# Kernel tuning notes

Hardware: AMD Instinct MI355X
Metric: run time of the kernel (lower is better)

The kernel has to match this reference:

```python
import jax, jax.numpy as jnp
import numpy as np

# dims matching init_kwargs
B, C, T = 64, 8, 2048
K, DIL = 16, 4            # kernel_size, dilation
MLP = 16                  # mlp_dim
NF = min(MLP, K // 2 + 1) # n_frequencies = 9
FEAT = C * NF * 2         # 144
H1, H2 = 64, 32           # ReLUBlock hidden dims (64 -> 64//2)
EFF = DIL * (K - 1)       # 60
W = T - EFF               # 1988 windows


def setup_inputs() -> dict:
    key = jax.random.key(0)
    ks = jax.random.split(key, 10)
    def lin(k, out_d, in_d):
        kw, kb = jax.random.split(k)
        bound = 1.0 / np.sqrt(in_d)
        w = jax.random.uniform(kw, (out_d, in_d), jnp.float32, -bound, bound)
        b = jax.random.uniform(kb, (out_d,), jnp.float32, -bound, bound)
        return w, b
    x = jax.random.normal(ks[0], (B, C, T), jnp.float32)
    proj_w, proj_b = lin(ks[1], MLP, FEAT)
    w1, b1 = lin(ks[2], H1, MLP)
    w2, b2 = lin(ks[3], H2, H1)
    out_w, out_b = lin(ks[4], 1, H2)
    agg_w = jax.random.normal(ks[5], (W,), jnp.float32) * 0.1
    return {"x": x, "proj_w": proj_w, "proj_b": proj_b, "w1": w1, "b1": b1,
            "w2": w2, "b2": b2, "out_w": out_w, "out_b": out_b, "agg_w": agg_w}


def reference(x, proj_w, proj_b, w1, b1, w2, b2, out_w, out_b, agg_w):
    # Build all dilated windows at once: window[t, j] = x[..., t - (K-1-j)*DIL]
    starts = jnp.arange(EFF, T)                      # [W]
    offs = -(K - 1 - jnp.arange(K)) * DIL            # [K]
    idx = starts[:, None] + offs[None, :]            # [W, K]
    win = x[:, :, idx]                               # [B, C, W, K]
    f = jnp.fft.rfft(win, axis=-1)[..., :NF]         # [B, C, W, NF]
    mag = jnp.log1p(jnp.abs(f))
    ph = jnp.angle(f) / jnp.pi
    feat = jnp.stack([mag, ph], axis=-1)             # [B, C, W, NF, 2]
    feat = feat.transpose(0, 2, 1, 3, 4).reshape(B, W, FEAT)  # [B, W, C*NF*2]
    p = jnp.tanh(feat @ proj_w.T + proj_b) * jnp.pi  # [B, W, MLP]
    h = jax.nn.relu(p @ w1.T + b1)                   # [B, W, H1]
    h = jax.nn.relu(h @ w2.T + b2)                   # [B, W, H2]
    out = (h @ out_w.T + out_b)[..., 0]              # [B, W]
    wts = jax.nn.softmax(agg_w)                      # [W]
    return (out * wts[None, :]).sum(axis=1)          # [B]
```

## Files before the change

### kernel.cpp

```cpp
#include <hip/hip_runtime.h>
#include <math.h>

#define B_    64
#define C_    8
#define T_    2048
#define K_    16
#define NF_   9
#define FEAT_ 144
#define MLP_  16
#define H1_   64
#define H2_   32
#define EFF_  60
#define W_    1988
#define NCHK_ 32
#define PI_F  3.14159265358979323846f
#define SPW   36
#define S1    20
#define S2    36

constexpr float COS16[16] = {
   1.0f,  0.92387953251128674f,  0.70710678118654752f,  0.38268343236508977f,
   0.0f, -0.38268343236508977f, -0.70710678118654752f, -0.92387953251128674f,
  -1.0f, -0.92387953251128674f, -0.70710678118654752f, -0.38268343236508977f,
   0.0f,  0.38268343236508977f,  0.70710678118654752f,  0.92387953251128674f };
constexpr float SIN16F[16] = {
   0.0f,  0.38268343236508977f,  0.70710678118654752f,  0.92387953251128674f,
   1.0f,  0.92387953251128674f,  0.70710678118654752f,  0.38268343236508977f,
   0.0f, -0.38268343236508977f, -0.70710678118654752f, -0.92387953251128674f,
  -1.0f, -0.92387953251128674f, -0.70710678118654752f, -0.38268343236508977f };

__device__ __forceinline__ float fast_log1p(float s) {
  return __builtin_amdgcn_logf(1.0f + s) * 0.69314718055994531f;
}

__device__ __forceinline__ float atanpi_poly(float r) {
  const float s2 = r * r;
  float p = -0.0037310f;
  p = fmaf(p, s2,  0.0167600f);
  p = fmaf(p, s2, -0.0370617f);
  p = fmaf(p, s2,  0.0616068f);
  p = fmaf(p, s2, -0.10587734f);
  p = fmaf(p, s2,  0.31830265f);
  return r * p;
}

__device__ __forceinline__ float atan2pi_fast(float im, float re) {
  const float ax = fabsf(re), ay = fabsf(im);
  const float mx = fmaxf(ax, ay), mn = fminf(ax, ay);
  const float r = mn * __builtin_amdgcn_rcpf(fmaxf(mx, 1e-37f));
  float t = atanpi_poly(r);
  t = (ay > ax) ? 0.5f - t : t;
  t = (__float_as_uint(re) & 0x80000000u) ? 1.0f - t : t;
  return copysignf(t, im);
}

__device__ __forceinline__ float fast_tanh(float z) {
  const float az = fabsf(z);
  const float e = __builtin_amdgcn_exp2f(-2.8853900817779268f * az);
  const float th = fmaf(-2.0f, e * __builtin_amdgcn_rcpf(1.0f + e), 1.0f);
  return copysignf(th, z);
}

__global__ __launch_bounds__(256) void setup_kernel(const float* __restrict__ agg,
                                                    float* __restrict__ wts,
                                                    const float* __restrict__ pw,
                                                    const float* __restrict__ w2,
                                                    float* __restrict__ PWt,
                                                    float* __restrict__ W2t) {
  if (blockIdx.x == 0) {
    __shared__ float red[256];
    const int tid = threadIdx.x;
    float m = -INFINITY;
    for (int i = tid; i < W_; i += 256) m = fmaxf(m, agg[i]);
    red[tid] = m; __syncthreads();
    for (int s = 128; s > 0; s >>= 1) { if (tid < s) red[tid] = fmaxf(red[tid], red[tid+s]); __syncthreads(); }
    const float mx = red[0];
    __syncthreads();
    float sum = 0.f;
    for (int i = tid; i < W_; i += 256) sum += expf(agg[i] - mx);
    red[tid] = sum; __syncthreads();
    for (int s = 128; s > 0; s >>= 1) { if (tid < s) red[tid] += red[tid+s]; __syncthreads(); }
    const float inv = 1.f / red[0];
    for (int i = tid; i < W_; i += 256) wts[i] = expf(agg[i] - mx) * inv;
  } else {
    const int tid = (blockIdx.x - 1) * 256 + threadIdx.x;
    if (tid < MLP_ * FEAT_) {
      const int j = tid / FEAT_, f = tid - j * FEAT_;
      PWt[f * MLP_ + j] = pw[tid];
    }
    if (tid < H2_ * H1_) {
      const int m = tid >> 6, i = tid & 63;
      W2t[i * H2_ + m] = w2[tid];
    }
  }
}

__global__ __launch_bounds__(256) void tcn_fused(
    const float* __restrict__ x,
    const float* __restrict__ PWt, const float* __restrict__ proj_b,
    const float* __restrict__ w1, const float* __restrict__ b1,
    const float* __restrict__ W2t, const float* __restrict__ b2,
    const float* __restrict__ out_w, const float* __restrict__ out_b,
    const float* __restrict__ wts, float* __restrict__ partials) {
  __shared__ __align__(16) float PWl[72 * SPW];
  __shared__ __align__(16) float W1p[H1_ * S1];
  __shared__ __align__(16) float W2p[H1_ * S2];
  __shared__ float B1s[H1_];

  const int tid = threadIdx.x;
  for (int idx = tid; idx < 72 * 32; idx += 256) { const int r = idx >> 5, j = idx & 31; PWl[r * SPW + j] = PWt[idx]; }
  for (int idx = tid; idx < H1_ * MLP_; idx += 256) { const int i = idx >> 4, j = idx & 15; W1p[i * S1 + j] = w1[idx]; }
  for (int idx = tid; idx < H1_ * H2_; idx += 256) { const int i = idx >> 5, m = idx & 31; W2p[i * S2 + m] = W2t[idx]; }
  if (tid < H1_) B1s[tid] = b1[tid];
  __syncthreads();

  const int lane = tid & 63;
  const int wave = tid >> 6;
  const int wloc = lane & 15;
  const int sub  = lane >> 4;
  const int b     = blockIdx.y;
  const int chunk = blockIdx.x;
  const int w  = chunk * 64 + wave * 16 + wloc;
  const int wl = (w < W_) ? w : (W_ - 1);

  float pacc[MLP_];
  #pragma unroll
  for (int j = 0; j < MLP_; j++) pacc[j] = 0.f;

  #pragma unroll
  for (int cc = 0; cc < 2; cc++) {
    const int c = sub * 2 + cc;
    const float* xc = x + ((size_t)b * C_ + c) * T_ + wl;
    float win[K_];
    #pragma unroll
    for (int k = 0; k < K_; k++) win[k] = xc[k * 4];
    float ae[8], bo[8];
    #pragma unroll
    for (int k = 0; k < 8; k++) { ae[k] = win[k] + win[k+8]; bo[k] = win[k] - win[k+8]; }

    #pragma unroll
    for (int n = 0; n < NF_; n++) {
      float re = 0.f, im = 0.f;
      #pragma unroll
      for (int k = 0; k < 8; k++) {
        const float v = (n & 1) ? bo[k] : ae[k];
        const int t = (n * k) & 15;
        re = fmaf(v,  COS16[t],  re);
        im = fmaf(v, -SIN16F[t], im);
      }
      const float s   = __builtin_amdgcn_sqrtf(fmaf(re, re, im * im));
      const float mag = fast_log1p(s);
      const float ph  = atan2pi_fast(im, re);
      const float4* rmv = reinterpret_cast<const float4*>(&PWl[(c * NF_ + n) * SPW]);
      #pragma unroll
      for (int q = 0; q < 4; q++) {
        const float4 a  = rmv[q];
        const float4 bb = rmv[q + 4];
        pacc[4*q+0] = fmaf(mag, a.x, fmaf(ph, bb.x, pacc[4*q+0]));
        pacc[4*q+1] = fmaf(mag, a.y, fmaf(ph, bb.y, pacc[4*q+1]));
        pacc[4*q+2] = fmaf(mag, a.z, fmaf(ph, bb.z, pacc[4*q+2]));
        pacc[4*q+3] = fmaf(mag, a.w, fmaf(ph, bb.w, pacc[4*q+3]));
      }
    }
  }

  #pragma unroll
  for (int j = 0; j < MLP_; j++) {
    pacc[j] += __shfl_xor(pacc[j], 16, 64);
    pacc[j] += __shfl_xor(pacc[j], 32, 64);
  }
  float p[MLP_];
  #pragma unroll
  for (int j = 0; j < MLP_; j++) p[j] = fast_tanh(pacc[j] + proj_b[j]) * PI_F;

  float h2a[H2_];
  #pragma unroll
  for (int m = 0; m < H2_; m++) h2a[m] = 0.f;
  #pragma unroll 4
  for (int ii = 0; ii < 16; ii++) {
    const int i = sub + ii * 4;
    const float4* r1 = reinterpret_cast<const float4*>(&W1p[i * S1]);
    float acc = B1s[i];
    #pragma unroll
    for (int q = 0; q < 4; q++) {
      const float4 a = r1[q];
      acc = fmaf(p[4*q+0], a.x, acc);
      acc = fmaf(p[4*q+1], a.y, acc);
      acc = fmaf(p[4*q+2], a.z, acc);
      acc = fmaf(p[4*q+3], a.w, acc);
    }
    const float h1v = fmaxf(acc, 0.f);
    const float4* r2 = reinterpret_cast<const float4*>(&W2p[i * S2]);
    #pragma unroll
    for (int q = 0; q < 8; q++) {
      const float4 a = r2[q];
      h2a[4*q+0] = fmaf(h1v, a.x, h2a[4*q+0]);
      h2a[4*q+1] = fmaf(h1v, a.y, h2a[4*q+1]);
      h2a[4*q+2] = fmaf(h1v, a.z, h2a[4*q+2]);
      h2a[4*q+3] = fmaf(h1v, a.w, h2a[4*q+3]);
    }
  }
  #pragma unroll
  for (int m = 0; m < H2_; m++) {
    h2a[m] += __shfl_xor(h2a[m], 16, 64);
    h2a[m] += __shfl_xor(h2a[m], 32, 64);
  }

  float o = out_b[0];
  #pragma unroll
  for (int m = 0; m < H2_; m++) o = fmaf(fmaxf(h2a[m] + b2[m], 0.f), out_w[m], o);
  float val = (sub == 0 && w < W_) ? o * wts[wl] : 0.f;
  #pragma unroll
  for (int s = 1; s < 64; s <<= 1) val += __shfl_xor(val, s, 64);
  if (lane == 0) partials[(b * NCHK_ + chunk) * 4 + wave] = val;
}

__global__ void finalize_kernel(const float* __restrict__ partials, float* __restrict__ out) {
  const int b = threadIdx.x;
  if (b < B_) {
    float s = 0.f;
    #pragma unroll 4
    for (int c = 0; c < NCHK_ * 4; c++) s += partials[b * NCHK_ * 4 + c];
    out[b] = s;
  }
}

extern "C" void kernel_launch(void* const* d_in, const int* in_sizes, int n_in,
                              void* d_out, int out_size, void* d_ws, size_t ws_size,
                              hipStream_t stream) {
  const float* x      = (const float*)d_in[0];
  const float* proj_w = (const float*)d_in[1];
  const float* proj_b = (const float*)d_in[2];
  const float* w1     = (const float*)d_in[3];
  const float* b1     = (const float*)d_in[4];
  const float* w2     = (const float*)d_in[5];
  const float* b2     = (const float*)d_in[6];
  const float* out_w  = (const float*)d_in[7];
  const float* out_b  = (const float*)d_in[8];
  const float* agg_w  = (const float*)d_in[9];

  float* wts      = (float*)d_ws;
  float* PWt      = (float*)d_ws + 2048;
  float* W2t      = (float*)d_ws + 2048 + 2304;
  float* partials = (float*)d_ws + 8192;

  setup_kernel<<<10, 256, 0, stream>>>(agg_w, wts, proj_w, w2, PWt, W2t);
  tcn_fused<<<dim3(NCHK_, B_), 256, 0, stream>>>(x, PWt, proj_b, w1, b1, W2t, b2,
                                                 out_w, out_b, wts, partials);
  finalize_kernel<<<1, 64, 0, stream>>>(partials, (float*)d_out);
}
```

Measured before the change: 59.79 us.

## Fuse setup into main kernel, use packed FMAs, special-case DC/Nyquist bins

Removes the separate setup kernel. Each block now transposes the projection and W2 weights from global memory into shared memory, and computes the softmax denominator itself with exp2 and no max subtraction. The MLP accumulations switch to packed two-wide float FMAs. The DC and Nyquist frequency bins are computed in closed form, with a sign-bit phase in place of atan2, and the final per-window dot product is split across sub-lanes. This saves a kernel launch and some ALU work, but every block now recomputes the softmax sum, and dropping the max subtraction risks overflow for large agg values.

```diff
diff --git a/kernel.cpp b/kernel.cpp
--- a/kernel.cpp
+++ b/kernel.cpp
@@ -14,9 +14,17 @@
 #define W_    1988
 #define NCHK_ 32
 #define PI_F  3.14159265358979323846f
+#define L2E_  1.44269504088896340736f
 #define SPW   36
 #define S1    20
 #define S2    36
+
+typedef float v2f __attribute__((ext_vector_type(2)));
+__device__ __forceinline__ v2f pkfma(v2f a, v2f b, v2f c) {
+  return __builtin_elementwise_fma(a, b, c);
+}
+__device__ __forceinline__ v2f lo2(float4 a) { v2f r; r.x = a.x; r.y = a.y; return r; }
+__device__ __forceinline__ v2f hi2(float4 a) { v2f r; r.x = a.z; r.y = a.w; return r; }
 
 constexpr float COS16[16] = {
    1.0f,  0.92387953251128674f,  0.70710678118654752f,  0.38268343236508977f,
@@ -32,7 +40,6 @@
 __device__ __forceinline__ float fast_log1p(float s) {
   return __builtin_amdgcn_logf(1.0f + s) * 0.69314718055994531f;
 }
-
 __device__ __forceinline__ float atanpi_poly(float r) {
   const float s2 = r * r;
   float p = -0.0037310f;
@@ -43,7 +50,6 @@
   p = fmaf(p, s2,  0.31830265f);
   return r * p;
 }
-
 __device__ __forceinline__ float atan2pi_fast(float im, float re) {
   const float ax = fabsf(re), ay = fabsf(im);
   const float mx = fmaxf(ax, ay), mn = fminf(ax, ay);
@@ -53,7 +59,6 @@
   t = (__float_as_uint(re) & 0x80000000u) ? 1.0f - t : t;
   return copysignf(t, im);
 }
-
 __device__ __forceinline__ float fast_tanh(float z) {
   const float az = fabsf(z);
   const float e = __builtin_amdgcn_exp2f(-2.8853900817779268f * az);
@@ -61,58 +66,42 @@
   return copysignf(th, z);
 }
 
-__global__ __launch_bounds__(256) void setup_kernel(const float* __restrict__ agg,
-                                                    float* __restrict__ wts,
-                                                    const float* __restrict__ pw,
-                                                    const float* __restrict__ w2,
-                                                    float* __restrict__ PWt,
-                                                    float* __restrict__ W2t) {
-  if (blockIdx.x == 0) {
-    __shared__ float red[256];
-    const int tid = threadIdx.x;
-    float m = -INFINITY;
-    for (int i = tid; i < W_; i += 256) m = fmaxf(m, agg[i]);
-    red[tid] = m; __syncthreads();
-    for (int s = 128; s > 0; s >>= 1) { if (tid < s) red[tid] = fmaxf(red[tid], red[tid+s]); __syncthreads(); }
-    const float mx = red[0];
-    __syncthreads();
-    float sum = 0.f;
-    for (int i = tid; i < W_; i += 256) sum += expf(agg[i] - mx);
-    red[tid] = sum; __syncthreads();
-    for (int s = 128; s > 0; s >>= 1) { if (tid < s) red[tid] += red[tid+s]; __syncthreads(); }
-    const float inv = 1.f / red[0];
-    for (int i = tid; i < W_; i += 256) wts[i] = expf(agg[i] - mx) * inv;
-  } else {
-    const int tid = (blockIdx.x - 1) * 256 + threadIdx.x;
-    if (tid < MLP_ * FEAT_) {
-      const int j = tid / FEAT_, f = tid - j * FEAT_;
-      PWt[f * MLP_ + j] = pw[tid];
-    }
-    if (tid < H2_ * H1_) {
-      const int m = tid >> 6, i = tid & 63;
-      W2t[i * H2_ + m] = w2[tid];
-    }
-  }
-}
-
-__global__ __launch_bounds__(256) void tcn_fused(
+__global__ __launch_bounds__(256) void tcn_all(
     const float* __restrict__ x,
-    const float* __restrict__ PWt, const float* __restrict__ proj_b,
+    const float* __restrict__ pw, const float* __restrict__ proj_b,
     const float* __restrict__ w1, const float* __restrict__ b1,
-    const float* __restrict__ W2t, const float* __restrict__ b2,
+    const float* __restrict__ w2, const float* __restrict__ b2,
     const float* __restrict__ out_w, const float* __restrict__ out_b,
-    const float* __restrict__ wts, float* __restrict__ partials) {
+    const float* __restrict__ agg, float* __restrict__ partials) {
   __shared__ __align__(16) float PWl[72 * SPW];
   __shared__ __align__(16) float W1p[H1_ * S1];
   __shared__ __align__(16) float W2p[H1_ * S2];
-  __shared__ float B1s[H1_];
+  __shared__ float B1s[H1_], B2s[H2_], OWs[H2_];
+  __shared__ float red[4];
 
   const int tid = threadIdx.x;
-  for (int idx = tid; idx < 72 * 32; idx += 256) { const int r = idx >> 5, j = idx & 31; PWl[r * SPW + j] = PWt[idx]; }
-  for (int idx = tid; idx < H1_ * MLP_; idx += 256) { const int i = idx >> 4, j = idx & 15; W1p[i * S1 + j] = w1[idx]; }
-  for (int idx = tid; idx < H1_ * H2_; idx += 256) { const int i = idx >> 5, m = idx & 31; W2p[i * S2 + m] = W2t[idx]; }
+  for (int idx = tid; idx < 72 * 32; idx += 256) {
+    const int r = idx >> 5, j32 = idx & 31, e = j32 >> 4, j = j32 & 15;
+    PWl[r * SPW + j32] = pw[j * FEAT_ + r * 2 + e];
+  }
+  for (int idx = tid; idx < H1_ * MLP_; idx += 256) {
+    const int i = idx >> 4, j = idx & 15;
+    W1p[i * S1 + j] = w1[idx];
+  }
+  for (int idx = tid; idx < H1_ * H2_; idx += 256) {
+    const int i = idx >> 5, m = idx & 31;
+    W2p[i * S2 + m] = w2[m * H1_ + i];
+  }
   if (tid < H1_) B1s[tid] = b1[tid];
+  if (tid < H2_) { B2s[tid] = b2[tid]; OWs[tid] = out_w[tid]; }
+
+  float se = 0.f;
+  for (int i = tid; i < W_; i += 256) se += __builtin_amdgcn_exp2f(agg[i] * L2E_);
+  #pragma unroll
+  for (int s = 1; s < 64; s <<= 1) se += __shfl_xor(se, s, 64);
+  if ((tid & 63) == 0) red[tid >> 6] = se;
   __syncthreads();
+  const float inv = 1.0f / ((red[0] + red[1]) + (red[2] + red[3]));
 
   const int lane = tid & 63;
   const int wave = tid >> 6;
@@ -123,9 +112,9 @@
   const int w  = chunk * 64 + wave * 16 + wloc;
   const int wl = (w < W_) ? w : (W_ - 1);
 
-  float pacc[MLP_];
-  #pragma unroll
-  for (int j = 0; j < MLP_; j++) pacc[j] = 0.f;
+  v2f pacc2[8];
+  #pragma unroll
+  for (int q = 0; q < 8; q++) pacc2[q] = (v2f){0.f, 0.f};
 
   #pragma unroll
   for (int cc = 0; cc < 2; cc++) {
@@ -138,8 +127,30 @@
     #pragma unroll
     for (int k = 0; k < 8; k++) { ae[k] = win[k] + win[k+8]; bo[k] = win[k] - win[k+8]; }
 
-    #pragma unroll
-    for (int n = 0; n < NF_; n++) {
+    {
+      const float r0 = ((ae[0]+ae[1])+(ae[2]+ae[3]))+((ae[4]+ae[5])+(ae[6]+ae[7]));
+      const float r8 = ((ae[0]-ae[1])+(ae[2]-ae[3]))+((ae[4]-ae[5])+(ae[6]-ae[7]));
+      const float mag0 = fast_log1p(fabsf(r0));
+      const float mag8 = fast_log1p(fabsf(r8));
+      const float ph0 = (__float_as_uint(r0) >> 31) ? 1.f : 0.f;
+      const float ph8 = (__float_as_uint(r8) >> 31) ? 1.f : 0.f;
+      const float4* rv0 = reinterpret_cast<const float4*>(&PWl[(c * NF_ + 0) * SPW]);
+      const float4* rv8 = reinterpret_cast<const float4*>(&PWl[(c * NF_ + 8) * SPW]);
+      const v2f mm0 = {mag0, mag0}, pp0 = {ph0, ph0};
+      const v2f mm8 = {mag8, mag8}, pp8 = {ph8, ph8};
+      #pragma unroll
+      for (int q = 0; q < 4; q++) {
+        const float4 a0 = rv0[q], b0 = rv0[q + 4];
+        const float4 a8 = rv8[q], b8 = rv8[q + 4];
+        pacc2[2*q]   = pkfma(mm0, lo2(a0), pkfma(pp0, lo2(b0), pacc2[2*q]));
+        pacc2[2*q+1] = pkfma(mm0, hi2(a0), pkfma(pp0, hi2(b0), pacc2[2*q+1]));
+        pacc2[2*q]   = pkfma(mm8, lo2(a8), pkfma(pp8, lo2(b8), pacc2[2*q]));
+        pacc2[2*q+1] = pkfma(mm8, hi2(a8), pkfma(pp8, hi2(b8), pacc2[2*q+1]));
+      }
+    }
+
+    #pragma unroll
+    for (int n = 1; n < 8; n++) {
       float re = 0.f, im = 0.f;
       #pragma unroll
       for (int k = 0; k < 8; k++) {
@@ -152,66 +163,81 @@
       const float mag = fast_log1p(s);
       const float ph  = atan2pi_fast(im, re);
       const float4* rmv = reinterpret_cast<const float4*>(&PWl[(c * NF_ + n) * SPW]);
+      const v2f mm = {mag, mag}, pp = {ph, ph};
       #pragma unroll
       for (int q = 0; q < 4; q++) {
         const float4 a  = rmv[q];
         const float4 bb = rmv[q + 4];
-        pacc[4*q+0] = fmaf(mag, a.x, fmaf(ph, bb.x, pacc[4*q+0]));
-        pacc[4*q+1] = fmaf(mag, a.y, fmaf(ph, bb.y, pacc[4*q+1]));
-        pacc[4*q+2] = fmaf(mag, a.z, fmaf(ph, bb.z, pacc[4*q+2]));
-        pacc[4*q+3] = fmaf(mag, a.w, fmaf(ph, bb.w, pacc[4*q+3]));
+        pacc2[2*q]   = pkfma(mm, lo2(a), pkfma(pp, lo2(bb), pacc2[2*q]));
+        pacc2[2*q+1] = pkfma(mm, hi2(a), pkfma(pp, hi2(bb), pacc2[2*q+1]));
       }
     }
   }
 
+  float* pf = reinterpret_cast<float*>(pacc2);
   #pragma unroll
   for (int j = 0; j < MLP_; j++) {
-    pacc[j] += __shfl_xor(pacc[j], 16, 64);
-    pacc[j] += __shfl_xor(pacc[j], 32, 64);
-  }
-  float p[MLP_];
-  #pragma unroll
-  for (int j = 0; j < MLP_; j++) p[j] = fast_tanh(pacc[j] + proj_b[j]) * PI_F;
-
-  float h2a[H2_];
-  #pragma unroll
-  for (int m = 0; m < H2_; m++) h2a[m] = 0.f;
+    pf[j] += __shfl_xor(pf[j], 16, 64);
+    pf[j] += __shfl_xor(pf[j], 32, 64);
+  }
+  v2f p2[8];
+  #pragma unroll
+  for (int q = 0; q < 8; q++) {
+    p2[q].x = fast_tanh(pf[2*q]   + proj_b[2*q])   * PI_F;
+    p2[q].y = fast_tanh(pf[2*q+1] + proj_b[2*q+1]) * PI_F;
+  }
+
+  v2f h2a2[16];
+  #pragma unroll
+  for (int q = 0; q < 16; q++) h2a2[q] = (v2f){0.f, 0.f};
   #pragma unroll 4
   for (int ii = 0; ii < 16; ii++) {
     const int i = sub + ii * 4;
     const float4* r1 = reinterpret_cast<const float4*>(&W1p[i * S1]);
-    float acc = B1s[i];
+    v2f acc2 = {0.f, 0.f};
     #pragma unroll
     for (int q = 0; q < 4; q++) {
       const float4 a = r1[q];
-      acc = fmaf(p[4*q+0], a.x, acc);
-      acc = fmaf(p[4*q+1], a.y, acc);
-      acc = fmaf(p[4*q+2], a.z, acc);
-      acc = fmaf(p[4*q+3], a.w, acc);
-    }
-    const float h1v = fmaxf(acc, 0.f);
+      acc2 = pkfma(p2[2*q],   lo2(a), acc2);
+      acc2 = pkfma(p2[2*q+1], hi2(a), acc2);
+    }
+    const float h1v = fmaxf(acc2.x + acc2.y + B1s[i], 0.f);
+    const v2f hh = {h1v, h1v};
     const float4* r2 = reinterpret_cast<const float4*>(&W2p[i * S2]);
     #pragma unroll
     for (int q = 0; q < 8; q++) {
       const float4 a = r2[q];
-      h2a[4*q+0] = fmaf(h1v, a.x, h2a[4*q+0]);
-      h2a[4*q+1] = fmaf(h1v, a.y, h2a[4*q+1]);
-      h2a[4*q+2] = fmaf(h1v, a.z, h2a[4*q+2]);
-      h2a[4*q+3] = fmaf(h1v, a.w, h2a[4*q+3]);
-    }
-  }
+      h2a2[2*q]   = pkfma(hh, lo2(a), h2a2[2*q]);
+      h2a2[2*q+1] = pkfma(hh, hi2(a), h2a2[2*q+1]);
+    }
+  }
+  float* hf = reinterpret_cast<float*>(h2a2);
   #pragma unroll
   for (int m = 0; m < H2_; m++) {
-    h2a[m] += __shfl_xor(h2a[m], 16, 64);
-    h2a[m] += __shfl_xor(h2a[m], 32, 64);
-  }
-
-  float o = out_b[0];
-  #pragma unroll
-  for (int m = 0; m < H2_; m++) o = fmaf(fmaxf(h2a[m] + b2[m], 0.f), out_w[m], o);
-  float val = (sub == 0 && w < W_) ? o * wts[wl] : 0.f;
-  #pragma unroll
-  for (int s = 1; s < 64; s <<= 1) val += __shfl_xor(val, s, 64);
+    hf[m] += __shfl_xor(hf[m], 16, 64);
+    hf[m] += __shfl_xor(hf[m], 32, 64);
+  }
+
+  v2f o2 = {0.f, 0.f};
+  #pragma unroll
+  for (int t = 0; t < 4; t++) {
+    const int pm = sub * 4 + t;
+    const v2f h = h2a2[pm];
+    v2f r;
+    r.x = fmaxf(h.x + B2s[2*pm],     0.f);
+    r.y = fmaxf(h.y + B2s[2*pm + 1], 0.f);
+    const v2f ow = {OWs[2*pm], OWs[2*pm + 1]};
+    o2 = pkfma(r, ow, o2);
+  }
+  float o = o2.x + o2.y;
+  o += __shfl_xor(o, 16, 64);
+  o += __shfl_xor(o, 32, 64);
+  o += out_b[0];
+
+  const float wv = __builtin_amdgcn_exp2f(agg[wl] * L2E_) * inv;
+  float val = (sub == 0 && w < W_) ? o * wv : 0.f;
+  #pragma unroll
+  for (int s = 1; s < 16; s <<= 1) val += __shfl_xor(val, s, 64);
   if (lane == 0) partials[(b * NCHK_ + chunk) * 4 + wave] = val;
 }
 
@@ -239,13 +265,9 @@
   const float* out_b  = (const float*)d_in[8];
   const float* agg_w  = (const float*)d_in[9];
 
-  float* wts      = (float*)d_ws;
-  float* PWt      = (float*)d_ws + 2048;
-  float* W2t      = (float*)d_ws + 2048 + 2304;
-  float* partials = (float*)d_ws + 8192;
-
-  setup_kernel<<<10, 256, 0, stream>>>(agg_w, wts, proj_w, w2, PWt, W2t);
-  tcn_fused<<<dim3(NCHK_, B_), 256, 0, stream>>>(x, PWt, proj_b, w1, b1, W2t, b2,
-                                                 out_w, out_b, wts, partials);
+  float* partials = (float*)d_ws;
+
+  tcn_all<<<dim3(NCHK_, B_), 256, 0, stream>>>(x, proj_w, proj_b, w1, b1, w2, b2,
+                                               out_w, out_b, agg_w, partials);
   finalize_kernel<<<1, 64, 0, stream>>>(partials, (float*)d_out);
 }
```

Measured after the change: 61.94 us. +3.6%, slower.

## Split work across 8 lanes per window, one channel per lane, 512-thread blocks

Applied to the files above, without the earlier changes.

Each window is now handled by 8 lanes, one per channel, instead of 4 lanes covering two channels each. Blocks grow to 512 threads with 8 waves of 8 windows. The DC and Nyquist bins are computed in closed form as real values, with phase taken from the sign. The MLP and output layers are split across the 8 lanes with an extra shuffle stage, and finalize now runs as 64 parallel blocks using wave reductions. This raises parallelism and shortens per-thread serial work, at the cost of more shuffles, higher register pressure per thread and a larger block.

```diff
diff --git a/kernel.cpp b/kernel.cpp
--- a/kernel.cpp
+++ b/kernel.cpp
@@ -32,7 +32,6 @@
 __device__ __forceinline__ float fast_log1p(float s) {
   return __builtin_amdgcn_logf(1.0f + s) * 0.69314718055994531f;
 }
-
 __device__ __forceinline__ float atanpi_poly(float r) {
   const float s2 = r * r;
   float p = -0.0037310f;
@@ -43,7 +42,6 @@
   p = fmaf(p, s2,  0.31830265f);
   return r * p;
 }
-
 __device__ __forceinline__ float atan2pi_fast(float im, float re) {
   const float ax = fabsf(re), ay = fabsf(im);
   const float mx = fmaxf(ax, ay), mn = fminf(ax, ay);
@@ -53,7 +51,6 @@
   t = (__float_as_uint(re) & 0x80000000u) ? 1.0f - t : t;
   return copysignf(t, im);
 }
-
 __device__ __forceinline__ float fast_tanh(float z) {
   const float az = fabsf(z);
   const float e = __builtin_amdgcn_exp2f(-2.8853900817779268f * az);
@@ -95,7 +92,7 @@
   }
 }
 
-__global__ __launch_bounds__(256) void tcn_fused(
+__global__ __launch_bounds__(512) void tcn_fused(
     const float* __restrict__ x,
     const float* __restrict__ PWt, const float* __restrict__ proj_b,
     const float* __restrict__ w1, const float* __restrict__ b1,
@@ -108,28 +105,27 @@
   __shared__ float B1s[H1_];
 
   const int tid = threadIdx.x;
-  for (int idx = tid; idx < 72 * 32; idx += 256) { const int r = idx >> 5, j = idx & 31; PWl[r * SPW + j] = PWt[idx]; }
-  for (int idx = tid; idx < H1_ * MLP_; idx += 256) { const int i = idx >> 4, j = idx & 15; W1p[i * S1 + j] = w1[idx]; }
-  for (int idx = tid; idx < H1_ * H2_; idx += 256) { const int i = idx >> 5, m = idx & 31; W2p[i * S2 + m] = W2t[idx]; }
+  for (int idx = tid; idx < 72 * 32; idx += 512) { const int r = idx >> 5, j = idx & 31; PWl[r * SPW + j] = PWt[idx]; }
+  for (int idx = tid; idx < H1_ * MLP_; idx += 512) { const int i = idx >> 4, j = idx & 15; W1p[i * S1 + j] = w1[idx]; }
+  for (int idx = tid; idx < H1_ * H2_; idx += 512) { const int i = idx >> 5, m = idx & 31; W2p[i * S2 + m] = W2t[idx]; }
   if (tid < H1_) B1s[tid] = b1[tid];
   __syncthreads();
 
   const int lane = tid & 63;
   const int wave = tid >> 6;
-  const int wloc = lane & 15;
-  const int sub  = lane >> 4;
+  const int wloc = lane & 7;
+  const int sub  = lane >> 3;
   const int b     = blockIdx.y;
   const int chunk = blockIdx.x;
-  const int w  = chunk * 64 + wave * 16 + wloc;
+  const int w  = chunk * 64 + wave * 8 + wloc;
   const int wl = (w < W_) ? w : (W_ - 1);
 
   float pacc[MLP_];
   #pragma unroll
   for (int j = 0; j < MLP_; j++) pacc[j] = 0.f;
 
-  #pragma unroll
-  for (int cc = 0; cc < 2; cc++) {
-    const int c = sub * 2 + cc;
+  {
+    const int c = sub;
     const float* xc = x + ((size_t)b * C_ + c) * T_ + wl;
     float win[K_];
     #pragma unroll
@@ -138,8 +134,32 @@
     #pragma unroll
     for (int k = 0; k < 8; k++) { ae[k] = win[k] + win[k+8]; bo[k] = win[k] - win[k+8]; }
 
-    #pragma unroll
-    for (int n = 0; n < NF_; n++) {
+    {
+      const float r0 = ((ae[0]+ae[1])+(ae[2]+ae[3]))+((ae[4]+ae[5])+(ae[6]+ae[7]));
+      const float r8 = ((ae[0]-ae[1])+(ae[2]-ae[3]))+((ae[4]-ae[5])+(ae[6]-ae[7]));
+      const float mag0 = fast_log1p(fabsf(r0));
+      const float mag8 = fast_log1p(fabsf(r8));
+      const float ph0 = (__float_as_uint(r0) >> 31) ? 1.f : 0.f;
+      const float ph8 = (__float_as_uint(r8) >> 31) ? 1.f : 0.f;
+      const float4* rv0 = reinterpret_cast<const float4*>(&PWl[(c * NF_ + 0) * SPW]);
+      const float4* rv8 = reinterpret_cast<const float4*>(&PWl[(c * NF_ + 8) * SPW]);
+      #pragma unroll
+      for (int q = 0; q < 4; q++) {
+        const float4 a0 = rv0[q], c0 = rv0[q + 4];
+        const float4 a8 = rv8[q], c8 = rv8[q + 4];
+        pacc[4*q+0] = fmaf(mag0, a0.x, fmaf(ph0, c0.x, pacc[4*q+0]));
+        pacc[4*q+1] = fmaf(mag0, a0.y, fmaf(ph0, c0.y, pacc[4*q+1]));
+        pacc[4*q+2] = fmaf(mag0, a0.z, fmaf(ph0, c0.z, pacc[4*q+2]));
+        pacc[4*q+3] = fmaf(mag0, a0.w, fmaf(ph0, c0.w, pacc[4*q+3]));
+        pacc[4*q+0] = fmaf(mag8, a8.x, fmaf(ph8, c8.x, pacc[4*q+0]));
+        pacc[4*q+1] = fmaf(mag8, a8.y, fmaf(ph8, c8.y, pacc[4*q+1]));
+        pacc[4*q+2] = fmaf(mag8, a8.z, fmaf(ph8, c8.z, pacc[4*q+2]));
+        pacc[4*q+3] = fmaf(mag8, a8.w, fmaf(ph8, c8.w, pacc[4*q+3]));
+      }
+    }
+
+    #pragma unroll
+    for (int n = 1; n < 8; n++) {
       float re = 0.f, im = 0.f;
       #pragma unroll
       for (int k = 0; k < 8; k++) {
@@ -166,6 +186,7 @@
 
   #pragma unroll
   for (int j = 0; j < MLP_; j++) {
+    pacc[j] += __shfl_xor(pacc[j], 8, 64);
     pacc[j] += __shfl_xor(pacc[j], 16, 64);
     pacc[j] += __shfl_xor(pacc[j], 32, 64);
   }
@@ -176,9 +197,9 @@
   float h2a[H2_];
   #pragma unroll
   for (int m = 0; m < H2_; m++) h2a[m] = 0.f;
-  #pragma unroll 4
-  for (int ii = 0; ii < 16; ii++) {
-    const int i = sub + ii * 4;
+  #pragma unroll
+  for (int ii = 0; ii < 8; ii++) {
+    const int i = sub + ii * 8;
     const float4* r1 = reinterpret_cast<const float4*>(&W1p[i * S1]);
     float acc = B1s[i];
     #pragma unroll
@@ -202,27 +223,38 @@
   }
   #pragma unroll
   for (int m = 0; m < H2_; m++) {
+    h2a[m] += __shfl_xor(h2a[m], 8, 64);
     h2a[m] += __shfl_xor(h2a[m], 16, 64);
     h2a[m] += __shfl_xor(h2a[m], 32, 64);
   }
 
-  float o = out_b[0];
-  #pragma unroll
-  for (int m = 0; m < H2_; m++) o = fmaf(fmaxf(h2a[m] + b2[m], 0.f), out_w[m], o);
+  float o = 0.f;
+  #pragma unroll
+  for (int t = 0; t < 4; t++) {
+    const int m = sub * 4 + t;
+    o = fmaf(fmaxf(h2a[m] + b2[m], 0.f), out_w[m], o);
+  }
+  o += __shfl_xor(o, 8, 64);
+  o += __shfl_xor(o, 16, 64);
+  o += __shfl_xor(o, 32, 64);
+  o += out_b[0];
+
   float val = (sub == 0 && w < W_) ? o * wts[wl] : 0.f;
-  #pragma unroll
-  for (int s = 1; s < 64; s <<= 1) val += __shfl_xor(val, s, 64);
-  if (lane == 0) partials[(b * NCHK_ + chunk) * 4 + wave] = val;
-}
-
-__global__ void finalize_kernel(const float* __restrict__ partials, float* __restrict__ out) {
-  const int b = threadIdx.x;
-  if (b < B_) {
-    float s = 0.f;
-    #pragma unroll 4
-    for (int c = 0; c < NCHK_ * 4; c++) s += partials[b * NCHK_ * 4 + c];
-    out[b] = s;
-  }
+  val += __shfl_xor(val, 1, 64);
+  val += __shfl_xor(val, 2, 64);
+  val += __shfl_xor(val, 4, 64);
+  if (lane == 0) partials[(b * NCHK_ + chunk) * 8 + wave] = val;
+}
+
+__global__ __launch_bounds__(64) void finalize_kernel(const float* __restrict__ partials,
+                                                      float* __restrict__ out) {
+  const int b = blockIdx.x;
+  const int l = threadIdx.x;
+  const float* pb = partials + b * NCHK_ * 8;
+  float s = ((pb[l] + pb[l + 64]) + (pb[l + 128] + pb[l + 192]));
+  #pragma unroll
+  for (int d = 1; d < 64; d <<= 1) s += __shfl_xor(s, d, 64);
+  if (l == 0) out[b] = s;
 }
 
 extern "C" void kernel_launch(void* const* d_in, const int* in_sizes, int n_in,
@@ -245,7 +277,7 @@
   float* partials = (float*)d_ws + 8192;
 
   setup_kernel<<<10, 256, 0, stream>>>(agg_w, wts, proj_w, w2, PWt, W2t);
-  tcn_fused<<<dim3(NCHK_, B_), 256, 0, stream>>>(x, PWt, proj_b, w1, b1, W2t, b2,
+  tcn_fused<<<dim3(NCHK_, B_), 512, 0, stream>>>(x, PWt, proj_b, w1, b1, W2t, b2,
                                                  out_w, out_b, wts, partials);
-  finalize_kernel<<<1, 64, 0, stream>>>(partials, (float*)d_out);
-}
+  finalize_kernel<<<B_, 64, 0, stream>>>(partials, (float*)d_out);
+}
```

Result: slower. 66.30 us (+10.9%).

## Use packed FP32 FMAs, special-case DC/Nyquist bins, split output dot across lanes

Applied to the files above, without the earlier changes.

The projection, first and second MLP layer accumulations now run through inline v_pk_fma_f32, processing two lanes of the accumulators per instruction. The DC and Nyquist frequency bins become real-only: they are computed with add trees, and their phase is taken from the sign bit, which avoids the complex DFT and the atan2 for those bins. The final out_w dot product is split across the four sub-lane groups and combined with shuffles, and the final window reduction is shortened to 16 lanes. The aim is to cut VALU instruction count. The risks are inline asm limiting compiler scheduling and extra shuffles or register moves.

```diff
diff --git a/kernel.cpp b/kernel.cpp
--- a/kernel.cpp
+++ b/kernel.cpp
@@ -18,6 +18,14 @@
 #define S1    20
 #define S2    36
 
+typedef float v2f __attribute__((ext_vector_type(2)));
+__device__ __forceinline__ void pkfma(v2f& acc, v2f a, v2f b) {
+  asm("v_pk_fma_f32 %0, %1, %2, %0" : "+v"(acc) : "v"(a), "v"(b));
+}
+__device__ __forceinline__ v2f mkv2(float x, float y) { v2f r; r.x = x; r.y = y; return r; }
+__device__ __forceinline__ v2f lo2(float4 a) { return mkv2(a.x, a.y); }
+__device__ __forceinline__ v2f hi2(float4 a) { return mkv2(a.z, a.w); }
+
 constexpr float COS16[16] = {
    1.0f,  0.92387953251128674f,  0.70710678118654752f,  0.38268343236508977f,
    0.0f, -0.38268343236508977f, -0.70710678118654752f, -0.92387953251128674f,
@@ -32,7 +40,6 @@
 __device__ __forceinline__ float fast_log1p(float s) {
   return __builtin_amdgcn_logf(1.0f + s) * 0.69314718055994531f;
 }
-
 __device__ __forceinline__ float atanpi_poly(float r) {
   const float s2 = r * r;
   float p = -0.0037310f;
@@ -43,7 +50,6 @@
   p = fmaf(p, s2,  0.31830265f);
   return r * p;
 }
-
 __device__ __forceinline__ float atan2pi_fast(float im, float re) {
   const float ax = fabsf(re), ay = fabsf(im);
   const float mx = fmaxf(ax, ay), mn = fminf(ax, ay);
@@ -53,7 +59,6 @@
   t = (__float_as_uint(re) & 0x80000000u) ? 1.0f - t : t;
   return copysignf(t, im);
 }
-
 __device__ __forceinline__ float fast_tanh(float z) {
   const float az = fabsf(z);
   const float e = __builtin_amdgcn_exp2f(-2.8853900817779268f * az);
@@ -123,9 +128,9 @@
   const int w  = chunk * 64 + wave * 16 + wloc;
   const int wl = (w < W_) ? w : (W_ - 1);
 
-  float pacc[MLP_];
-  #pragma unroll
-  for (int j = 0; j < MLP_; j++) pacc[j] = 0.f;
+  v2f pacc2[8];
+  #pragma unroll
+  for (int q = 0; q < 8; q++) pacc2[q] = mkv2(0.f, 0.f);
 
   #pragma unroll
   for (int cc = 0; cc < 2; cc++) {
@@ -138,8 +143,30 @@
     #pragma unroll
     for (int k = 0; k < 8; k++) { ae[k] = win[k] + win[k+8]; bo[k] = win[k] - win[k+8]; }
 
-    #pragma unroll
-    for (int n = 0; n < NF_; n++) {
+    {
+      const float r0 = ((ae[0]+ae[1])+(ae[2]+ae[3]))+((ae[4]+ae[5])+(ae[6]+ae[7]));
+      const float r8 = ((ae[0]-ae[1])+(ae[2]-ae[3]))+((ae[4]-ae[5])+(ae[6]-ae[7]));
+      const float mag0 = fast_log1p(fabsf(r0));
+      const float mag8 = fast_log1p(fabsf(r8));
+      const float ph0 = (__float_as_uint(r0) >> 31) ? 1.f : 0.f;
+      const float ph8 = (__float_as_uint(r8) >> 31) ? 1.f : 0.f;
+      const float4* rv0 = reinterpret_cast<const float4*>(&PWl[(c * NF_ + 0) * SPW]);
+      const float4* rv8 = reinterpret_cast<const float4*>(&PWl[(c * NF_ + 8) * SPW]);
+      const v2f mm0 = mkv2(mag0, mag0), pp0 = mkv2(ph0, ph0);
+      const v2f mm8 = mkv2(mag8, mag8), pp8 = mkv2(ph8, ph8);
+      #pragma unroll
+      for (int q = 0; q < 4; q++) {
+        const float4 a0 = rv0[q], c0 = rv0[q + 4];
+        const float4 a8 = rv8[q], c8 = rv8[q + 4];
+        pkfma(pacc2[2*q],   mm0, lo2(a0));  pkfma(pacc2[2*q],   pp0, lo2(c0));
+        pkfma(pacc2[2*q+1], mm0, hi2(a0));  pkfma(pacc2[2*q+1], pp0, hi2(c0));
+        pkfma(pacc2[2*q],   mm8, lo2(a8));  pkfma(pacc2[2*q],   pp8, lo2(c8));
+        pkfma(pacc2[2*q+1], mm8, hi2(a8));  pkfma(pacc2[2*q+1], pp8, hi2(c8));
+      }
+    }
+
+    #pragma unroll
+    for (int n = 1; n < 8; n++) {
       float re = 0.f, im = 0.f;
       #pragma unroll
       for (int k = 0; k < 8; k++) {
@@ -152,66 +179,74 @@
       const float mag = fast_log1p(s);
       const float ph  = atan2pi_fast(im, re);
       const float4* rmv = reinterpret_cast<const float4*>(&PWl[(c * NF_ + n) * SPW]);
+      const v2f mm = mkv2(mag, mag), pp = mkv2(ph, ph);
       #pragma unroll
       for (int q = 0; q < 4; q++) {
         const float4 a  = rmv[q];
         const float4 bb = rmv[q + 4];
-        pacc[4*q+0] = fmaf(mag, a.x, fmaf(ph, bb.x, pacc[4*q+0]));
-        pacc[4*q+1] = fmaf(mag, a.y, fmaf(ph, bb.y, pacc[4*q+1]));
-        pacc[4*q+2] = fmaf(mag, a.z, fmaf(ph, bb.z, pacc[4*q+2]));
-        pacc[4*q+3] = fmaf(mag, a.w, fmaf(ph, bb.w, pacc[4*q+3]));
+        pkfma(pacc2[2*q],   mm, lo2(a));  pkfma(pacc2[2*q],   pp, lo2(bb));
+        pkfma(pacc2[2*q+1], mm, hi2(a));  pkfma(pacc2[2*q+1], pp, hi2(bb));
       }
     }
   }
 
+  float* pf = reinterpret_cast<float*>(pacc2);
   #pragma unroll
   for (int j = 0; j < MLP_; j++) {
-    pacc[j] += __shfl_xor(pacc[j], 16, 64);
-    pacc[j] += __shfl_xor(pacc[j], 32, 64);
-  }
-  float p[MLP_];
-  #pragma unroll
-  for (int j = 0; j < MLP_; j++) p[j] = fast_tanh(pacc[j] + proj_b[j]) * PI_F;
-
-  float h2a[H2_];
-  #pragma unroll
-  for (int m = 0; m < H2_; m++) h2a[m] = 0.f;
+    pf[j] += __shfl_xor(pf[j], 16, 64);
+    pf[j] += __shfl_xor(pf[j], 32, 64);
+  }
+  v2f p2[8];
+  #pragma unroll
+  for (int q = 0; q < 8; q++) {
+    p2[q] = mkv2(fast_tanh(pf[2*q]   + proj_b[2*q])   * PI_F,
+                 fast_tanh(pf[2*q+1] + proj_b[2*q+1]) * PI_F);
+  }
+
+  v2f h2a2[16];
+  #pragma unroll
+  for (int q = 0; q < 16; q++) h2a2[q] = mkv2(0.f, 0.f);
   #pragma unroll 4
   for (int ii = 0; ii < 16; ii++) {
     const int i = sub + ii * 4;
     const float4* r1 = reinterpret_cast<const float4*>(&W1p[i * S1]);
-    float acc = B1s[i];
+    v2f acc2 = mkv2(B1s[i], 0.f);
     #pragma unroll
     for (int q = 0; q < 4; q++) {
       const float4 a = r1[q];
-      acc = fmaf(p[4*q+0], a.x, acc);
-      acc = fmaf(p[4*q+1], a.y, acc);
-      acc = fmaf(p[4*q+2], a.z, acc);
-      acc = fmaf(p[4*q+3], a.w, acc);
-    }
-    const float h1v = fmaxf(acc, 0.f);
+      pkfma(acc2, p2[2*q],   lo2(a));
+      pkfma(acc2, p2[2*q+1], hi2(a));
+    }
+    const float h1v = fmaxf(acc2.x + acc2.y, 0.f);
+    const v2f hh = mkv2(h1v, h1v);
     const float4* r2 = reinterpret_cast<const float4*>(&W2p[i * S2]);
     #pragma unroll
     for (int q = 0; q < 8; q++) {
       const float4 a = r2[q];
-      h2a[4*q+0] = fmaf(h1v, a.x, h2a[4*q+0]);
-      h2a[4*q+1] = fmaf(h1v, a.y, h2a[4*q+1]);
-      h2a[4*q+2] = fmaf(h1v, a.z, h2a[4*q+2]);
-      h2a[4*q+3] = fmaf(h1v, a.w, h2a[4*q+3]);
-    }
-  }
+      pkfma(h2a2[2*q],   hh, lo2(a));
+      pkfma(h2a2[2*q+1], hh, hi2(a));
+    }
+  }
+  float* hf = reinterpret_cast<float*>(h2a2);
   #pragma unroll
   for (int m = 0; m < H2_; m++) {
-    h2a[m] += __shfl_xor(h2a[m], 16, 64);
-    h2a[m] += __shfl_xor(h2a[m], 32, 64);
-  }
-
-  float o = out_b[0];
-  #pragma unroll
-  for (int m = 0; m < H2_; m++) o = fmaf(fmaxf(h2a[m] + b2[m], 0.f), out_w[m], o);
+    hf[m] += __shfl_xor(hf[m], 16, 64);
+    hf[m] += __shfl_xor(hf[m], 32, 64);
+  }
+
+  float o = 0.f;
+  #pragma unroll
+  for (int t = 0; t < 8; t++) {
+    const int m = sub * 8 + t;
+    o = fmaf(fmaxf(hf[m] + b2[m], 0.f), out_w[m], o);
+  }
+  o += __shfl_xor(o, 16, 64);
+  o += __shfl_xor(o, 32, 64);
+  o += out_b[0];
+
   float val = (sub == 0 && w < W_) ? o * wts[wl] : 0.f;
   #pragma unroll
-  for (int s = 1; s < 64; s <<= 1) val += __shfl_xor(val, s, 64);
+  for (int s = 1; s < 16; s <<= 1) val += __shfl_xor(val, s, 64);
   if (lane == 0) partials[(b * NCHK_ + chunk) * 4 + wave] = val;
 }
 
```

Result: faster. 58.02 us (-3.0%).
